# Kernel optimization log

Hardware: AMD Instinct MI355X
Metric: run time of the kernel (lower is better)

Reference implementation:

```python
import jax, jax.numpy as jnp
import numpy as np

N_NODES = 100000
NUM_REL = 2


def rgcn_conv(x, src, dst, etype, W, root, bias):
    """PyG-style RGCNConv: per-relation mean aggregation + root transform + bias.
    x: [N, in], W: [R, in, out], root: [in, out], bias: [out].
    """
    R = W.shape[0]
    N = x.shape[0]
    # Pre-transform nodes by every relation weight: [R, N, out]
    xr = jnp.einsum('ni,rio->rno', x, W)
    msgs = xr[etype, src]  # [E, out] gather per-edge, relation-typed
    seg_id = dst * R + etype  # combined (node, relation) segment id
    summed = jax.ops.segment_sum(msgs, seg_id, num_segments=N * R)
    cnt = jax.ops.segment_sum(jnp.ones(etype.shape, x.dtype), seg_id, num_segments=N * R)
    summed = summed.reshape(N, R, -1)
    cnt = cnt.reshape(N, R, 1)
    agg = (summed / jnp.maximum(cnt, 1.0)).sum(axis=1)  # sum over relations of per-relation means
    return agg + x @ root + bias


def setup_inputs() -> dict:
    key = jax.random.key(0)
    ks = jax.random.split(key, 9)
    d = 128
    E = 800000
    sc = 1.0 / np.sqrt(d)
    return {
        'x': jax.random.normal(ks[0], (N_NODES, d), jnp.float32),
        'edge_index_a': jax.random.randint(ks[1], (2, E), 0, N_NODES, jnp.int64),
        'edge_index_b': jax.random.randint(ks[2], (2, E), 0, N_NODES, jnp.int64),
        'W1': jax.random.normal(ks[3], (NUM_REL, d, d), jnp.float32) * sc,
        'root1': jax.random.normal(ks[4], (d, d), jnp.float32) * sc,
        'b1': jnp.zeros((d,), jnp.float32),
        'W2': jax.random.normal(ks[5], (NUM_REL, d, d), jnp.float32) * sc,
        'root2': jax.random.normal(ks[6], (d, d), jnp.float32) * sc,
        'b2': jnp.zeros((d,), jnp.float32),
    }


def reference(x, edge_index_a, edge_index_b, W1, root1, b1, W2, root2, b2):
    # Concatenate per-relation edge lists + build edge_type ids (a->0, b->1)
    edge_index = jnp.concatenate([edge_index_a, edge_index_b], axis=1)
    etype = jnp.concatenate([
        jnp.zeros((edge_index_a.shape[1],), jnp.int32),
        jnp.ones((edge_index_b.shape[1],), jnp.int32),
    ])
    src, dst = edge_index[0], edge_index[1]
    h = rgcn_conv(x, src, dst, etype, W1, root1, b1)
    h = jax.nn.relu(h)
    out = rgcn_conv(h, src, dst, etype, W2, root2, b2)
    return out
```

## Files before the change

### kernel.cpp

```cpp
#include <hip/hip_runtime.h>
#include <hip/hip_bf16.h>


typedef __attribute__((ext_vector_type(8))) short bf16x8;
typedef __attribute__((ext_vector_type(4))) float f32x4;
typedef unsigned short ushort_t;
typedef unsigned int uint_t;

#define BSHIFT 9
#define SEGB (1 << (BSHIFT + 1))
#define NBMAX 256
#define SLAB 16384
#define CH_PER_THREAD 8
#define CHUNK (256 * CH_PER_THREAD)

#define GBM 256
#define KCH 128
#define LDBE 136

#define ROWB 768
#define XOFF 512

__device__ __forceinline__ ushort_t f2b(float f) {
  union { float f; uint_t u; } v;
  v.f = f;
  uint_t u = v.u;
  return (ushort_t)((u + 0x7FFFu + ((u >> 16) & 1u)) >> 16);
}
__device__ __forceinline__ void dot2acc(float& a, uint_t pk, uint_t sel) {
  asm("v_dot2_f32_bf16 %0, %1, %2, %0" : "+v"(a) : "v"(pk), "v"(sel));
}

__global__ __launch_bounds__(256) void prep(
    const float* __restrict__ W1, const float* __restrict__ root1,
    const float* __restrict__ W2, const float* __restrict__ root2,
    ushort_t* __restrict__ Bt1, ushort_t* __restrict__ Bt2,
    const float* __restrict__ x, ushort_t* __restrict__ aggbuf1, int N) {
  int b = blockIdx.x;
  if (b < 384) {
    int flat = b * 256 + threadIdx.x;
    int which = flat >= 49152;
    int idx = flat - which * 49152;
    int c = idx / 384;
    int k = idx - c * 384;
    const float* W = which ? W2 : W1;
    const float* root = which ? root2 : root1;
    ushort_t* Bt = which ? Bt2 : Bt1;
    float v = (k < 256) ? W[(size_t)k * 128 + c] : root[(size_t)(k - 256) * 128 + c];
    Bt[(size_t)c * 384 + k] = f2b(v);
  } else {
    int idx = (b - 384) * 256 + threadIdx.x;
    int n = idx >> 6, lane = idx & 63;
    if (n < N) {
      float2 v = *(const float2*)(x + (size_t)n * 128 + lane * 2);
      uint_t pk = (uint_t)f2b(v.x) | ((uint_t)f2b(v.y) << 16);
      *(uint_t*)(aggbuf1 + (size_t)n * 384 + 256 + lane * 2) = pk;
    }
  }
}

__global__ __launch_bounds__(256) void bucket_bin(
    const int* __restrict__ ea, const int* __restrict__ eb,
    int E, int NB, int* __restrict__ cursor, uint_t* __restrict__ staging) {
  __shared__ int h[NBMAX];
  __shared__ int bbase[NBMAX];
  int t = threadIdx.x;
  for (int i = t; i < NB; i += 256) h[i] = 0;
  __syncthreads();

  int tbase = blockIdx.x * CHUNK + t;
  int total = 2 * E;
  uint_t val[CH_PER_THREAD];
  short bktv[CH_PER_THREAD];
#pragma unroll
  for (int j = 0; j < CH_PER_THREAD; ++j) {
    int i = tbase + j * 256;
    if (i < total) {
      int src, dst, rel;
      if (i < E) { src = ea[i];     dst = ea[E + i]; rel = 0; }
      else       { src = eb[i - E]; dst = eb[i];     rel = 1; }
      int seg = dst * 2 + rel;
      int bkt = seg >> (BSHIFT + 1);
      val[j] = ((uint_t)src << 10) | (uint_t)(seg & (SEGB - 1));
      bktv[j] = (short)bkt;
      atomicAdd(&h[bkt], 1);
    } else {
      bktv[j] = -1;
    }
  }
  __syncthreads();
  for (int i = t; i < NB; i += 256) {
    int c = h[i];
    bbase[i] = c ? i * SLAB + atomicAdd(&cursor[i], c) : 0;
    h[i] = 0;
  }
  __syncthreads();
#pragma unroll
  for (int j = 0; j < CH_PER_THREAD; ++j) {
    if (bktv[j] >= 0) {
      int bkt = bktv[j];
      int r = atomicAdd(&h[bkt], 1);
      staging[(size_t)bbase[bkt] + r] = val[j];
    }
  }
}

__global__ __launch_bounds__(256) void bucket_build(
    const uint_t* __restrict__ staging, const int* __restrict__ cursor,
    int* __restrict__ csr, int* __restrict__ offs,
    int* __restrict__ ends, int nseg) {
  __shared__ int scnt[SEGB];
  __shared__ int sexcl[SEGB];
  __shared__ int sdata[256];
  int b = blockIdx.x;
  int t = threadIdx.x;
  int base = b * SLAB;
  int ne = cursor[b];
  int seg0 = b << (BSHIFT + 1);

  for (int i = t; i < SEGB; i += 256) scnt[i] = 0;
  __syncthreads();
  const uint_t* st = staging + base;
  for (int i = t; i < ne; i += 256) {
    atomicAdd(&scnt[st[i] & (SEGB - 1)], 1);
  }
  __syncthreads();
  int c0 = scnt[t * 4 + 0], c1 = scnt[t * 4 + 1];
  int c2 = scnt[t * 4 + 2], c3 = scnt[t * 4 + 3];
  int s = c0 + c1 + c2 + c3;
  sdata[t] = s;
  __syncthreads();
  for (int off = 1; off < 256; off <<= 1) {
    int tmp = (t >= off) ? sdata[t - off] : 0;
    __syncthreads();
    sdata[t] += tmp;
    __syncthreads();
  }
  int excl = sdata[t] - s;
  int e0 = excl, e1 = excl + c0, e2 = e1 + c1, e3 = e2 + c2;
  sexcl[t * 4 + 0] = e0;
  sexcl[t * 4 + 1] = e1;
  sexcl[t * 4 + 2] = e2;
  sexcl[t * 4 + 3] = e3;
  {
    int g = seg0 + t * 4;
    if (g + 0 < nseg) { offs[g + 0] = base + e0; ends[g + 0] = base + e0 + c0; }
    if (g + 1 < nseg) { offs[g + 1] = base + e1; ends[g + 1] = base + e1 + c1; }
    if (g + 2 < nseg) { offs[g + 2] = base + e2; ends[g + 2] = base + e2 + c2; }
    if (g + 3 < nseg) { offs[g + 3] = base + e3; ends[g + 3] = base + e3 + c3; }
  }
  scnt[t * 4 + 0] = 0;
  scnt[t * 4 + 1] = 0;
  scnt[t * 4 + 2] = 0;
  scnt[t * 4 + 3] = 0;
  __syncthreads();
  for (int i = t; i < ne; i += 256) {
    uint_t rec = st[i];
    int seg = (int)(rec & (SEGB - 1));
    int src = (int)(rec >> 10);
    int r = atomicAdd(&scnt[seg], 1);
    csr[base + sexcl[seg] + r] = src * ROWB + XOFF;
  }
}

#define ACC8(v)                                            \
  dot2acc(acc[0], v.x, sel_lo); dot2acc(acc[1], v.x, sel_hi); \
  dot2acc(acc[2], v.y, sel_lo); dot2acc(acc[3], v.y, sel_hi); \
  dot2acc(acc[4], v.z, sel_lo); dot2acc(acc[5], v.z, sel_hi); \
  dot2acc(acc[6], v.w, sel_lo); dot2acc(acc[7], v.w, sel_hi);

__global__ __launch_bounds__(256) void agg_kernel(
    const char* __restrict__ xbc,
    const int* __restrict__ csr,
    const int* __restrict__ offs, const int* __restrict__ ends,
    ushort_t* __restrict__ agg, int nseg) {
  int wid = (blockIdx.x * blockDim.x + threadIdx.x) >> 6;
  if (wid >= nseg) return;
  int lane = threadIdx.x & 63;
  int q = lane >> 4;
  int t = lane & 15;
  int beg = offs[wid], end = ends[wid];
  const uint_t sel_lo = 0x00003F80u;
  const uint_t sel_hi = 0x3F800000u;

  float acc[8];
#pragma unroll
  for (int j = 0; j < 8; ++j) acc[j] = 0.f;

  const char* xt = xbc + t * 16;
  int e = beg + q;
  for (; e + 12 < end; e += 16) {
    int o0 = csr[e];
    int o1 = csr[e + 4];
    int o2 = csr[e + 8];
    int o3 = csr[e + 12];
    uint4 v0 = *(const uint4*)(xt + o0);
    uint4 v1 = *(const uint4*)(xt + o1);
    uint4 v2 = *(const uint4*)(xt + o2);
    uint4 v3 = *(const uint4*)(xt + o3);
    ACC8(v0); ACC8(v1); ACC8(v2); ACC8(v3);
  }
  for (; e < end; e += 4) {
    int o0 = csr[e];
    uint4 v0 = *(const uint4*)(xt + o0);
    ACC8(v0);
  }

#pragma unroll
  for (int j = 0; j < 8; ++j) {
    acc[j] += __shfl_xor(acc[j], 16);
    acc[j] += __shfl_xor(acc[j], 32);
  }

  int c = end - beg;
  float inv = 1.0f / (float)(c > 1 ? c : 1);
  if (q == 0) {
    uint4 o;
    o.x = (uint_t)f2b(acc[0] * inv) | ((uint_t)f2b(acc[1] * inv) << 16);
    o.y = (uint_t)f2b(acc[2] * inv) | ((uint_t)f2b(acc[3] * inv) << 16);
    o.z = (uint_t)f2b(acc[4] * inv) | ((uint_t)f2b(acc[5] * inv) << 16);
    o.w = (uint_t)f2b(acc[6] * inv) | ((uint_t)f2b(acc[7] * inv) << 16);
    int n = wid >> 1, r = wid & 1;
    *(uint4*)(agg + (size_t)n * 384 + r * 128 + t * 8) = o;
  }
}

__device__ __forceinline__ void do_mfma32(
    const char* bs, f32x4 (&acc)[4][8], const bf16x8 (&a)[4],
    int ks, int lrow, int kg) {
  bf16x8 b[8];
#pragma unroll
  for (int c = 0; c < 8; ++c)
    b[c] = *(const bf16x8*)(bs + (c * 16 + lrow) * (LDBE * 2) +
                            (ks * 4 + kg) * 16);
#pragma unroll
  for (int r = 0; r < 4; ++r)
#pragma unroll
    for (int c = 0; c < 8; ++c)
      acc[r][c] = __builtin_amdgcn_mfma_f32_16x16x32_bf16(a[r], b[c], acc[r][c], 0, 0, 0);
}

template <int MODE>
__global__ __launch_bounds__(256, 2) void mfma_gemm(
    const ushort_t* __restrict__ A,
    const ushort_t* __restrict__ Bt,
    const float* __restrict__ bias,
    float* __restrict__ outf,
    ushort_t* __restrict__ outb,
    int M) {
  __shared__ __align__(16) ushort_t Bs[2][128 * LDBE];
  const int tid = threadIdx.x;
  const int lane = tid & 63;
  const int wave = tid >> 6;
  const int lrow = lane & 15;
  const int kg = lane >> 4;
  const int rowbase = blockIdx.x * GBM + wave * 64;

  f32x4 acc[4][8];
#pragma unroll
  for (int r = 0; r < 4; ++r)
#pragma unroll
    for (int c = 0; c < 8; ++c) acc[r][c] = (f32x4){0.f, 0.f, 0.f, 0.f};

  uint4 stg[8];
#pragma unroll
  for (int j = 0; j < 8; ++j) {
    int flat = tid + j * 256;
    int col = flat >> 4;
    int q = flat & 15;
    stg[j] = *(const uint4*)(Bt + (size_t)col * 384 + q * 8);
  }
#pragma unroll
  for (int j = 0; j < 8; ++j) {
    int flat = tid + j * 256;
    int col = flat >> 4;
    int q = flat & 15;
    *(uint4*)((char*)&Bs[0][0] + col * (LDBE * 2) + q * 16) = stg[j];
  }
  __syncthreads();

  int cur = 0;
  for (int ch = 0; ch < 3; ++ch) {
    if (ch < 2) {
#pragma unroll
      for (int j = 0; j < 8; ++j) {
        int flat = tid + j * 256;
        int col = flat >> 4;
        int q = flat & 15;
        stg[j] = *(const uint4*)(Bt + (size_t)col * 384 + (ch + 1) * KCH + q * 8);
      }
    }
    const ushort_t* ab = A + (size_t)ch * KCH + kg * 8;
    const char* bsbase = (const char*)&Bs[0][0] + cur * (128 * LDBE * 2);
    bf16x8 aA[4], aB[4];
#pragma unroll
    for (int r = 0; r < 4; ++r)
      aA[r] = *(const bf16x8*)(ab + (size_t)(rowbase + r * 16 + lrow) * 384);
#pragma unroll
    for (int r = 0; r < 4; ++r)
      aB[r] = *(const bf16x8*)(ab + (size_t)(rowbase + r * 16 + lrow) * 384 + 32);
    do_mfma32(bsbase, acc, aA, 0, lrow, kg);
#pragma unroll
    for (int r = 0; r < 4; ++r)
      aA[r] = *(const bf16x8*)(ab + (size_t)(rowbase + r * 16 + lrow) * 384 + 64);
    do_mfma32(bsbase, acc, aB, 1, lrow, kg);
#pragma unroll
    for (int r = 0; r < 4; ++r)
      aB[r] = *(const bf16x8*)(ab + (size_t)(rowbase + r * 16 + lrow) * 384 + 96);
    do_mfma32(bsbase, acc, aA, 2, lrow, kg);
    do_mfma32(bsbase, acc, aB, 3, lrow, kg);
    if (ch < 2) {
#pragma unroll
      for (int j = 0; j < 8; ++j) {
        int flat = tid + j * 256;
        int col = flat >> 4;
        int q = flat & 15;
        *(uint4*)((char*)&Bs[0][0] + (cur ^ 1) * (128 * LDBE * 2) +
                  col * (LDBE * 2) + q * 16) = stg[j];
      }
      __syncthreads();
      cur ^= 1;
    }
  }

#pragma unroll
  for (int c = 0; c < 8; ++c) {
    int col = c * 16 + lrow;
    float bv = bias[col];
#pragma unroll
    for (int r = 0; r < 4; ++r) {
      int r0 = rowbase + r * 16 + kg * 4;
#pragma unroll
      for (int j = 0; j < 4; ++j) {
        int row = r0 + j;
        if (row < M) {
          float v = acc[r][c][j] + bv;
          if (MODE == 1) {
            v = fmaxf(v, 0.f);
            outb[(size_t)row * 384 + 256 + col] = f2b(v);
          } else {
            outf[(size_t)row * 128 + col] = v;
          }
        }
      }
    }
  }
}

extern "C" void kernel_launch(void* const* d_in, const int* in_sizes, int n_in,
                              void* d_out, int out_size, void* d_ws, size_t ws_size,
                              hipStream_t stream) {
  const float* x     = (const float*)d_in[0];
  const int*   ea    = (const int*)d_in[1];
  const int*   eb    = (const int*)d_in[2];
  const float* W1    = (const float*)d_in[3];
  const float* root1 = (const float*)d_in[4];
  const float* b1    = (const float*)d_in[5];
  const float* W2    = (const float*)d_in[6];
  const float* root2 = (const float*)d_in[7];
  const float* b2    = (const float*)d_in[8];
  float* out = (float*)d_out;

  const int N = in_sizes[0] / 128;
  const int E = in_sizes[1] / 2;
  const int nseg = N * 2;
  const int Mblk = (N + GBM - 1) / GBM;
  const int Mpad = Mblk * GBM;
  const int NB = ((N - 1) >> BSHIFT) + 1;
  const int nchunk = (2 * E + CHUNK - 1) / CHUNK;
  const int XSB = (N * 64 + 255) / 256;

  char* p = (char*)d_ws;
  ushort_t* aggbuf1 = (ushort_t*)p;  p += (size_t)Mpad * 384 * sizeof(ushort_t);
  ushort_t* aggbuf2 = (ushort_t*)p;  p += (size_t)Mpad * 384 * sizeof(ushort_t);
  ushort_t* Bt1 = (ushort_t*)p;      p += (size_t)128 * 384 * sizeof(ushort_t);
  ushort_t* Bt2 = (ushort_t*)p;      p += (size_t)128 * 384 * sizeof(ushort_t);
  int* csr = (int*)p;                p += (size_t)NBMAX * SLAB * sizeof(int);
  int* offs = (int*)p;               p += (size_t)nseg * sizeof(int);
  int* ends = (int*)p;               p += (size_t)nseg * sizeof(int);
  int* cursor = (int*)p;             p += NBMAX * sizeof(int);
  uint_t* staging = (uint_t*)aggbuf2;

  hipMemsetAsync(cursor, 0, NBMAX * sizeof(int), stream);

  prep<<<384 + XSB, 256, 0, stream>>>(
      W1, root1, W2, root2, Bt1, Bt2, x, aggbuf1, N);

  bucket_bin<<<nchunk, 256, 0, stream>>>(ea, eb, E, NB, cursor, staging);
  bucket_build<<<NB, 256, 0, stream>>>(staging, cursor, csr, offs, ends, nseg);

  const int agg_blocks = (nseg + 3) / 4;

  agg_kernel<<<agg_blocks, 256, 0, stream>>>((const char*)aggbuf1, csr, offs,
                                             ends, aggbuf1, nseg);
  mfma_gemm<1><<<Mblk, 256, 0, stream>>>(aggbuf1, Bt1, b1, nullptr, aggbuf2, N);

  agg_kernel<<<agg_blocks, 256, 0, stream>>>((const char*)aggbuf2, csr, offs,
                                             ends, aggbuf2, nseg);
  mfma_gemm<0><<<Mblk, 256, 0, stream>>>(aggbuf2, Bt2, b2, out, nullptr, N);
}
```

Before: 335.4 us.

## Coalesce bucket staging writes via LDS sort, stage GEMM bf16 epilogue, shrink agg unroll

The binning kernel now does a block-wide prefix scan over bucket counts. It sorts each chunk's records by bucket in shared memory and writes them to staging in contiguous runs instead of scattered single stores. The layer-1 GEMM epilogue writes ReLU'd bf16 results into LDS per wave and then emits 16-byte row-contiguous stores instead of 2-byte scattered ones. The aggregation loop's unroll drops from 4 edges to 2 per iteration, trading memory-level parallelism for lower register pressure. The new LDS arrays add 16KB+ to the binning kernel, and the epilogue reuses the Bs buffer, which must be large enough for 4 waves × 64×128 bf16.

```diff
diff --git a/kernel.cpp b/kernel.cpp
--- a/kernel.cpp
+++ b/kernel.cpp
@@ -64,6 +64,10 @@
     int E, int NB, int* __restrict__ cursor, uint_t* __restrict__ staging) {
   __shared__ int h[NBMAX];
   __shared__ int bbase[NBMAX];
+  __shared__ int lofs[NBMAX];
+  __shared__ int sscan[256];
+  __shared__ uint_t sval[CHUNK];
+  __shared__ int sdst[CHUNK];
   int t = threadIdx.x;
   for (int i = t; i < NB; i += 256) h[i] = 0;
   __syncthreads();
@@ -89,20 +93,39 @@
     }
   }
   __syncthreads();
-  for (int i = t; i < NB; i += 256) {
-    int c = h[i];
-    bbase[i] = c ? i * SLAB + atomicAdd(&cursor[i], c) : 0;
-    h[i] = 0;
-  }
+  {
+    int v = (t < NB) ? h[t] : 0;
+    sscan[t] = v;
+    __syncthreads();
+    for (int off = 1; off < 256; off <<= 1) {
+      int tmp = (t >= off) ? sscan[t - off] : 0;
+      __syncthreads();
+      sscan[t] += tmp;
+      __syncthreads();
+    }
+    if (t < NB) {
+      lofs[t] = sscan[t] - v;
+      bbase[t] = v ? t * SLAB + atomicAdd(&cursor[t], v) : 0;
+    }
+  }
+  __syncthreads();
+  for (int i = t; i < NB; i += 256) h[i] = 0;
   __syncthreads();
 #pragma unroll
   for (int j = 0; j < CH_PER_THREAD; ++j) {
     if (bktv[j] >= 0) {
       int bkt = bktv[j];
       int r = atomicAdd(&h[bkt], 1);
-      staging[(size_t)bbase[bkt] + r] = val[j];
-    }
-  }
+      int pos = lofs[bkt] + r;
+      sval[pos] = val[j];
+      sdst[pos] = bbase[bkt] + r;
+    }
+  }
+  __syncthreads();
+  int nrec = total - blockIdx.x * CHUNK;
+  if (nrec > CHUNK) nrec = CHUNK;
+  for (int i = t; i < nrec; i += 256)
+    staging[sdst[i]] = sval[i];
 }
 
 __global__ __launch_bounds__(256) void bucket_build(
@@ -162,12 +185,6 @@
     csr[base + sexcl[seg] + r] = src * ROWB + XOFF;
   }
 }
-
-#define ACC8(v)                                            \
-  dot2acc(acc[0], v.x, sel_lo); dot2acc(acc[1], v.x, sel_hi); \
-  dot2acc(acc[2], v.y, sel_lo); dot2acc(acc[3], v.y, sel_hi); \
-  dot2acc(acc[4], v.z, sel_lo); dot2acc(acc[5], v.z, sel_hi); \
-  dot2acc(acc[6], v.w, sel_lo); dot2acc(acc[7], v.w, sel_hi);
 
 __global__ __launch_bounds__(256) void agg_kernel(
     const char* __restrict__ xbc,
@@ -189,21 +206,27 @@
 
   const char* xt = xbc + t * 16;
   int e = beg + q;
-  for (; e + 12 < end; e += 16) {
+  for (; e + 4 < end; e += 8) {
     int o0 = csr[e];
     int o1 = csr[e + 4];
-    int o2 = csr[e + 8];
-    int o3 = csr[e + 12];
     uint4 v0 = *(const uint4*)(xt + o0);
     uint4 v1 = *(const uint4*)(xt + o1);
-    uint4 v2 = *(const uint4*)(xt + o2);
-    uint4 v3 = *(const uint4*)(xt + o3);
-    ACC8(v0); ACC8(v1); ACC8(v2); ACC8(v3);
-  }
-  for (; e < end; e += 4) {
+    dot2acc(acc[0], v0.x, sel_lo); dot2acc(acc[1], v0.x, sel_hi);
+    dot2acc(acc[2], v0.y, sel_lo); dot2acc(acc[3], v0.y, sel_hi);
+    dot2acc(acc[4], v0.z, sel_lo); dot2acc(acc[5], v0.z, sel_hi);
+    dot2acc(acc[6], v0.w, sel_lo); dot2acc(acc[7], v0.w, sel_hi);
+    dot2acc(acc[0], v1.x, sel_lo); dot2acc(acc[1], v1.x, sel_hi);
+    dot2acc(acc[2], v1.y, sel_lo); dot2acc(acc[3], v1.y, sel_hi);
+    dot2acc(acc[4], v1.z, sel_lo); dot2acc(acc[5], v1.z, sel_hi);
+    dot2acc(acc[6], v1.w, sel_lo); dot2acc(acc[7], v1.w, sel_hi);
+  }
+  if (e < end) {
     int o0 = csr[e];
     uint4 v0 = *(const uint4*)(xt + o0);
-    ACC8(v0);
+    dot2acc(acc[0], v0.x, sel_lo); dot2acc(acc[1], v0.x, sel_hi);
+    dot2acc(acc[2], v0.y, sel_lo); dot2acc(acc[3], v0.y, sel_hi);
+    dot2acc(acc[4], v0.z, sel_lo); dot2acc(acc[5], v0.z, sel_hi);
+    dot2acc(acc[6], v0.w, sel_lo); dot2acc(acc[7], v0.w, sel_hi);
   }
 
 #pragma unroll
@@ -323,23 +346,45 @@
     }
   }
 
-#pragma unroll
-  for (int c = 0; c < 8; ++c) {
-    int col = c * 16 + lrow;
-    float bv = bias[col];
-#pragma unroll
-    for (int r = 0; r < 4; ++r) {
-      int r0 = rowbase + r * 16 + kg * 4;
-#pragma unroll
-      for (int j = 0; j < 4; ++j) {
-        int row = r0 + j;
-        if (row < M) {
-          float v = acc[r][c][j] + bv;
-          if (MODE == 1) {
-            v = fmaxf(v, 0.f);
-            outb[(size_t)row * 384 + 256 + col] = f2b(v);
-          } else {
-            outf[(size_t)row * 128 + col] = v;
+  if (MODE == 1) {
+    __syncthreads();
+    ushort_t* ws = (ushort_t*)&Bs[0][0] + wave * (64 * 128);
+#pragma unroll
+    for (int c = 0; c < 8; ++c) {
+      int col = c * 16 + lrow;
+      float bv = bias[col];
+#pragma unroll
+      for (int r = 0; r < 4; ++r)
+#pragma unroll
+        for (int j = 0; j < 4; ++j) {
+          float v = fmaxf(acc[r][c][j] + bv, 0.f);
+          ws[(r * 16 + kg * 4 + j) * 128 + col] = f2b(v);
+        }
+    }
+    __syncthreads();
+#pragma unroll
+    for (int rr = 0; rr < 16; ++rr) {
+      int lr = rr * 4 + (lane >> 4);
+      int row = rowbase + lr;
+      int tq = lane & 15;
+      if (row < M) {
+        uint4 v = *(const uint4*)(ws + lr * 128 + tq * 8);
+        *(uint4*)(outb + (size_t)row * 384 + 256 + tq * 8) = v;
+      }
+    }
+  } else {
+#pragma unroll
+    for (int c = 0; c < 8; ++c) {
+      int col = c * 16 + lrow;
+      float bv = bias[col];
+#pragma unroll
+      for (int r = 0; r < 4; ++r) {
+        int r0 = rowbase + r * 16 + kg * 4;
+#pragma unroll
+        for (int j = 0; j < 4; ++j) {
+          int row = r0 + j;
+          if (row < M) {
+            outf[(size_t)row * 128 + col] = acc[r][c][j] + bv;
           }
         }
       }
```

Result: faster. 308.0 us (-8.2%).
